# Kernel optimization log

Measured on AMD Instinct MI355X. Metric: run time of the kernel, lower is better.

Reference implementation:

```python
import jax, jax.numpy as jnp
import numpy as np

N_NODES = 100000
D_IN = 256
D_HID = 64
D_EMB = 32
ADJ_NNZ = 3200000
N_EDGES = 2000000


def setup_inputs() -> dict:
    key = jax.random.key(0)
    ks = jax.random.split(key, 8)
    x = jax.random.normal(ks[0], (N_NODES, D_IN), dtype=jnp.float32)
    adj_src = jax.random.randint(ks[1], (ADJ_NNZ,), 0, N_NODES, dtype=jnp.int32)
    adj_dst = jax.random.randint(ks[2], (ADJ_NNZ,), 0, N_NODES, dtype=jnp.int32)
    adj_val = jax.random.uniform(ks[3], (ADJ_NNZ,), dtype=jnp.float32)
    edge_index = jax.random.randint(ks[4], (2, N_EDGES), 0, N_NODES, dtype=jnp.int32)
    # Xavier-uniform weights, zero biases (matches reset_parameters)
    lim1 = float(np.sqrt(6.0 / (D_IN + D_HID)))
    lim2 = float(np.sqrt(6.0 / (D_HID + D_EMB)))
    W1 = jax.random.uniform(ks[5], (D_IN, D_HID), minval=-lim1, maxval=lim1, dtype=jnp.float32)
    b1 = jnp.zeros((D_HID,), dtype=jnp.float32)
    W2 = jax.random.uniform(ks[6], (D_HID, D_EMB), minval=-lim2, maxval=lim2, dtype=jnp.float32)
    b2 = jnp.zeros((D_EMB,), dtype=jnp.float32)
    return {"x": x, "adj_src": adj_src, "adj_dst": adj_dst, "adj_val": adj_val,
            "edge_index": edge_index, "W1": W1, "b1": b1, "W2": W2, "b2": b2}


def _spmm(adj_src, adj_dst, adj_val, dense):
    # (sparse A) @ dense : out[i] = sum_{e: dst[e]==i} val[e] * dense[src[e]]
    n = dense.shape[0]
    msgs = adj_val[:, None] * dense[adj_src]            # [nnz, d]
    return jax.ops.segment_sum(msgs, adj_dst, num_segments=n)


def reference(x, adj_src, adj_dst, adj_val, edge_index, W1, b1, W2, b2):
    # Layer 1: ReLU(A_norm @ (x W1) + b1)
    z1 = jax.nn.relu(_spmm(adj_src, adj_dst, adj_val, x @ W1) + b1)
    # Layer 2: A_norm @ (z1 W2) + b2 (no activation)
    z2 = _spmm(adj_src, adj_dst, adj_val, z1 @ W2) + b2   # [n, d_emb]
    # Inner-product decoder over edges
    src, dst = edge_index[0], edge_index[1]
    scores = jnp.sum(z2[src] * z2[dst], axis=1)          # [num_edges]
    return scores
```

## Files before the change

### kernel.cpp

```cpp
#include <hip/hip_runtime.h>
#include <hip/hip_bf16.h>


#define D_IN  256
#define D_HID 64
#define D_EMB 32
#define BROWS 256
#define NBUK_MAX 512
#define TILE  4096
#define PBS   512
#define SBS   1024

typedef unsigned short u16;
typedef unsigned int u32;
typedef __attribute__((ext_vector_type(8))) short short8;
typedef __attribute__((ext_vector_type(4))) float f32x4;

__device__ __forceinline__ float bf2f(u32 u) {
  return __uint_as_float((u & 0xFFFFu) << 16);
}
__device__ __forceinline__ float bf2f_hi(u32 u) {
  return __uint_as_float(u & 0xFFFF0000u);
}
__device__ __forceinline__ u16 f2bf(float f) {
  u32 x = __float_as_uint(f);
  x += 0x7FFFu + ((x >> 16) & 1u);
  return (u16)(x >> 16);
}
__device__ __forceinline__ void unpack8(uint4 u, float* f) {
  f[0] = bf2f(u.x); f[1] = bf2f(u.x >> 16);
  f[2] = bf2f(u.y); f[3] = bf2f(u.y >> 16);
  f[4] = bf2f(u.z); f[5] = bf2f(u.z >> 16);
  f[6] = bf2f(u.w); f[7] = bf2f(u.w >> 16);
}

__global__ __launch_bounds__(256) void w1_swizzle_kernel(
    const float* __restrict__ W1, uint4* __restrict__ gswz) {
  const int s = blockIdx.x * 256 + threadIdx.x;
  const int lane = s & 63;
  const int kstep = (s >> 6) & 7;
  const int nt = s >> 9;
  const int col = nt * 16 + (lane & 15);
  const int kbase = kstep * 32 + (lane >> 4) * 8;
  u32 p[4];
  for (int jp = 0; jp < 4; ++jp) {
    u32 lo = f2bf(W1[(kbase + 2 * jp) * D_HID + col]);
    u32 hi = f2bf(W1[(kbase + 2 * jp + 1) * D_HID + col]);
    p[jp] = lo | (hi << 16);
  }
  gswz[s] = make_uint4(p[0], p[1], p[2], p[3]);
}

__global__ __launch_bounds__(256) void gemm1_mfma_kernel(
    const float* __restrict__ x, const uint4* __restrict__ gswz,
    u16* __restrict__ h1, int M) {
  const int tid = threadIdx.x;
  const int wv = tid >> 6;
  const int lane = tid & 63;
  const int quad = lane >> 4;
  const int m = lane & 15;

  const int rowbase = blockIdx.x * 64 + wv * 16;
  int arow = rowbase + m;
  if (arow >= M) arow = M - 1;

  f32x4 acc[4];
  for (int nt = 0; nt < 4; ++nt) acc[nt] = (f32x4){0.f, 0.f, 0.f, 0.f};

  const float* xrow = &x[(long long)arow * D_IN];

#pragma unroll
  for (int kstep = 0; kstep < 8; ++kstep) {
    const int kbase = kstep * 32 + quad * 8;
    float4 a0 = *(const float4*)&xrow[kbase];
    float4 a1 = *(const float4*)&xrow[kbase + 4];
    short8 af;
    af[0] = (short)f2bf(a0.x); af[1] = (short)f2bf(a0.y);
    af[2] = (short)f2bf(a0.z); af[3] = (short)f2bf(a0.w);
    af[4] = (short)f2bf(a1.x); af[5] = (short)f2bf(a1.y);
    af[6] = (short)f2bf(a1.z); af[7] = (short)f2bf(a1.w);
#pragma unroll
    for (int nt = 0; nt < 4; ++nt) {
      uint4 bu = gswz[(nt * 8 + kstep) * 64 + lane];
      short8 bf = *(short8*)&bu;
      acc[nt] = __builtin_amdgcn_mfma_f32_16x16x32_bf16(af, bf, acc[nt], 0, 0, 0);
    }
  }

#pragma unroll
  for (int nt = 0; nt < 4; ++nt) {
#pragma unroll
    for (int r = 0; r < 4; ++r) {
      int orow = rowbase + quad * 4 + r;
      if (orow < M)
        h1[(long long)orow * D_HID + nt * 16 + m] = f2bf(acc[nt][r]);
    }
  }
}

__global__ __launch_bounds__(256) void bin_count(
    const int* __restrict__ dst, int* __restrict__ hist, int nnz, int nbuk) {
  __shared__ int h[NBUK_MAX];
  for (int i = threadIdx.x; i < nbuk; i += 256) h[i] = 0;
  __syncthreads();
  const int stride = gridDim.x * 256;
  for (int e = blockIdx.x * 256 + threadIdx.x; e < nnz; e += stride)
    atomicAdd(&h[dst[e] >> 8], 1);
  __syncthreads();
  for (int i = threadIdx.x; i < nbuk; i += 256) {
    int v = h[i];
    if (v) atomicAdd(&hist[i], v);
  }
}

__global__ __launch_bounds__(256) void bin_scan(
    int* __restrict__ hist, int* __restrict__ cur, int n) {
  __shared__ int sm[256];
  const int t = threadIdx.x;
  const int per = (n + 255) / 256;
  const int base = t * per;
  int loc[4];
  int s = 0;
  for (int i = 0; i < per; ++i) {
    int idx = base + i;
    int v = (idx < n) ? hist[idx] : 0;
    loc[i] = s;
    s += v;
  }
  sm[t] = s;
  __syncthreads();
  for (int off = 1; off < 256; off <<= 1) {
    int tmp = (t >= off) ? sm[t - off] : 0;
    __syncthreads();
    sm[t] += tmp;
    __syncthreads();
  }
  const int b0 = sm[t] - s;
  for (int i = 0; i < per; ++i) {
    int idx = base + i;
    if (idx < n) {
      int p = b0 + loc[i];
      hist[idx] = p;
      cur[idx] = p;
    }
  }
  if (t == 255) hist[n] = sm[255];
}

__global__ __launch_bounds__(PBS) void partition_kernel(
    const int* __restrict__ src, const int* __restrict__ dst,
    const float* __restrict__ val, int* __restrict__ cur,
    int2* __restrict__ payload, int nnz, int nbuk) {
  __shared__ int2 stage[TILE];
  __shared__ int hist[NBUK_MAX];
  __shared__ int lcur[NBUK_MAX];
  __shared__ int gbase[NBUK_MAX];
  __shared__ int sm[PBS];

  const int t = threadIdx.x;
  const long long base = (long long)blockIdx.x * TILE;
  const int cnt = min(TILE, (int)(nnz - base));

  for (int i = t; i < nbuk; i += PBS) hist[i] = 0;
  __syncthreads();

  constexpr int PER = TILE / PBS;
  int key[PER], vq[PER];
  short bk[PER];
  for (int i = 0; i < PER; ++i) {
    int idx = t + i * PBS;
    if (idx < cnt) {
      int d = dst[base + idx];
      int b = d >> 8;
      bk[i] = (short)b;
      key[i] = (src[base + idx] << 8) | (d & (BROWS - 1));
      int q = (int)(val[base + idx] * 32768.f + 0.5f);
      q = min(q, 32767);
      vq[i] = (b << 15) | q;
      atomicAdd(&hist[b], 1);
    } else {
      bk[i] = -1;
    }
  }
  __syncthreads();

  {
    int c = (t < nbuk) ? hist[t] : 0;
    sm[t] = c;
    __syncthreads();
    for (int off = 1; off < PBS; off <<= 1) {
      int tmp = (t >= off) ? sm[t - off] : 0;
      __syncthreads();
      sm[t] += tmp;
      __syncthreads();
    }
    int excl = sm[t] - c;
    if (t < nbuk) {
      hist[t] = excl;
      lcur[t] = excl;
      if (c > 0) gbase[t] = atomicAdd(&cur[t], c);
    }
  }
  __syncthreads();

  for (int i = 0; i < PER; ++i) {
    if (bk[i] >= 0) {
      int p = atomicAdd(&lcur[bk[i]], 1);
      stage[p] = make_int2(key[i], vq[i]);
    }
  }
  __syncthreads();

  for (int i = t; i < cnt; i += PBS) {
    int2 pk = stage[i];
    int b = pk.y >> 15;
    payload[gbase[b] + (i - hist[b])] = pk;
  }
}

__global__ __launch_bounds__(SBS) void bucket_sort_kernel(
    const int* __restrict__ bscan, const int2* __restrict__ payload,
    u32* __restrict__ csr, int* __restrict__ rs, int M) {
  __shared__ int cnt_s[BROWS];
  __shared__ int sm[BROWS];
  const int b = blockIdx.x;
  const int t = threadIdx.x;
  const int start = bscan[b];
  const int end = bscan[b + 1];

  if (t < BROWS) cnt_s[t] = 0;
  __syncthreads();
  for (int j = start + t; j < end; j += SBS)
    atomicAdd(&cnt_s[payload[j].x & (BROWS - 1)], 1);
  __syncthreads();

  int v = 0;
  if (t < BROWS) { v = cnt_s[t]; sm[t] = v; }
  __syncthreads();
  for (int off = 1; off < BROWS; off <<= 1) {
    int tmp = 0;
    if (t < BROWS && t >= off) tmp = sm[t - off];
    __syncthreads();
    if (t < BROWS) sm[t] += tmp;
    __syncthreads();
  }
  if (t < BROWS) {
    int row = b * BROWS + t;
    if (row < M) rs[row] = start + sm[t];
    cnt_s[t] = start + sm[t] - v;
  }
  __syncthreads();

  for (int j = start + t; j < end; j += SBS) {
    int2 pk = payload[j];
    int r = pk.x & (BROWS - 1);
    int p = atomicAdd(&cnt_s[r], 1);
    csr[p] = ((u32)(pk.x >> 8) << 15) | (u32)(pk.y & 32767);
  }
}

template <int D, bool RELU>
__global__ __launch_bounds__(256) void spmm_csr_kernel(
    const int* __restrict__ rs, const u32* __restrict__ csr,
    const u16* __restrict__ in, const float* __restrict__ bias,
    u16* __restrict__ out, int M) {
  constexpr int TEAM = D / 4;
  const int lt = threadIdx.x % TEAM;
  const int row = blockIdx.x * (256 / TEAM) + threadIdx.x / TEAM;
  if (row >= M) return;
  const int start = (row == 0) ? 0 : rs[row - 1];
  const int end = rs[row];
  const float qs = 1.f / 32768.f;
  const u16* inp = in + lt * 4;

  float a0 = 0.f, a1 = 0.f, a2 = 0.f, a3 = 0.f;
  int j = start;
  for (; j + 4 <= end; j += 4) {
    u32 p0 = csr[j], p1 = csr[j + 1], p2 = csr[j + 2], p3 = csr[j + 3];
    uint2 w0 = *(const uint2*)&inp[(long long)(p0 >> 15) * D];
    uint2 w1 = *(const uint2*)&inp[(long long)(p1 >> 15) * D];
    uint2 w2 = *(const uint2*)&inp[(long long)(p2 >> 15) * D];
    uint2 w3 = *(const uint2*)&inp[(long long)(p3 >> 15) * D];
    float v0 = (float)(p0 & 32767u) * qs;
    float v1 = (float)(p1 & 32767u) * qs;
    float v2 = (float)(p2 & 32767u) * qs;
    float v3 = (float)(p3 & 32767u) * qs;
    a0 = fmaf(v0, bf2f(w0.x), a0); a1 = fmaf(v0, bf2f_hi(w0.x), a1);
    a2 = fmaf(v0, bf2f(w0.y), a2); a3 = fmaf(v0, bf2f_hi(w0.y), a3);
    a0 = fmaf(v1, bf2f(w1.x), a0); a1 = fmaf(v1, bf2f_hi(w1.x), a1);
    a2 = fmaf(v1, bf2f(w1.y), a2); a3 = fmaf(v1, bf2f_hi(w1.y), a3);
    a0 = fmaf(v2, bf2f(w2.x), a0); a1 = fmaf(v2, bf2f_hi(w2.x), a1);
    a2 = fmaf(v2, bf2f(w2.y), a2); a3 = fmaf(v2, bf2f_hi(w2.y), a3);
    a0 = fmaf(v3, bf2f(w3.x), a0); a1 = fmaf(v3, bf2f_hi(w3.x), a1);
    a2 = fmaf(v3, bf2f(w3.y), a2); a3 = fmaf(v3, bf2f_hi(w3.y), a3);
  }
  for (; j < end; ++j) {
    u32 pk = csr[j];
    uint2 w = *(const uint2*)&inp[(long long)(pk >> 15) * D];
    float v = (float)(pk & 32767u) * qs;
    a0 = fmaf(v, bf2f(w.x), a0); a1 = fmaf(v, bf2f_hi(w.x), a1);
    a2 = fmaf(v, bf2f(w.y), a2); a3 = fmaf(v, bf2f_hi(w.y), a3);
  }
  const float4 bv = *(const float4*)&bias[lt * 4];
  a0 += bv.x; a1 += bv.y; a2 += bv.z; a3 += bv.w;
  if (RELU) {
    a0 = fmaxf(a0, 0.f); a1 = fmaxf(a1, 0.f);
    a2 = fmaxf(a2, 0.f); a3 = fmaxf(a3, 0.f);
  }
  uint2 o;
  o.x = (u32)f2bf(a0) | ((u32)f2bf(a1) << 16);
  o.y = (u32)f2bf(a2) | ((u32)f2bf(a3) << 16);
  *(uint2*)&out[(long long)row * D + lt * 4] = o;
}

__global__ __launch_bounds__(256) void gemm2_kernel(
    const u16* __restrict__ z1, const float* __restrict__ W2,
    u16* __restrict__ h2, int M) {
  __shared__ float ws[D_HID * D_EMB];
  const int tid = threadIdx.x;
  for (int i = tid; i < D_HID * D_EMB / 4; i += 256)
    ((float4*)ws)[i] = ((const float4*)W2)[i];
  __syncthreads();

  const int row = blockIdx.x * 256 + tid;
  if (row >= M) return;

  float4 acc4[8];
  for (int c = 0; c < 8; ++c) acc4[c] = make_float4(0.f, 0.f, 0.f, 0.f);

  const uint4* zr = (const uint4*)&z1[(long long)row * D_HID];
  for (int blk = 0; blk < 8; ++blk) {
    float a8[8];
    unpack8(zr[blk], a8);
    for (int kk = 0; kk < 8; ++kk) {
      const float a = a8[kk];
      const float4* wr = (const float4*)&ws[(blk * 8 + kk) * D_EMB];
      for (int c = 0; c < 8; ++c) {
        float4 wv = wr[c];
        acc4[c].x += a * wv.x;
        acc4[c].y += a * wv.y;
        acc4[c].z += a * wv.z;
        acc4[c].w += a * wv.w;
      }
    }
  }
  u32 pk[16];
  for (int c = 0; c < 8; ++c) {
    pk[c * 2 + 0] = (u32)f2bf(acc4[c].x) | ((u32)f2bf(acc4[c].y) << 16);
    pk[c * 2 + 1] = (u32)f2bf(acc4[c].z) | ((u32)f2bf(acc4[c].w) << 16);
  }
  uint4* op = (uint4*)&h2[(long long)row * D_EMB];
  op[0] = make_uint4(pk[0], pk[1], pk[2], pk[3]);
  op[1] = make_uint4(pk[4], pk[5], pk[6], pk[7]);
  op[2] = make_uint4(pk[8], pk[9], pk[10], pk[11]);
  op[3] = make_uint4(pk[12], pk[13], pk[14], pk[15]);
}

__global__ __launch_bounds__(256) void decode_kernel(
    const int* __restrict__ ei, const u16* __restrict__ z2,
    float* __restrict__ out, int nE) {
  const int e = blockIdx.x * 256 + threadIdx.x;
  if (e >= nE) return;
  const int s = ei[e];
  const int d = ei[nE + e];
  const uint4* za = (const uint4*)&z2[(long long)s * D_EMB];
  const uint4* zb = (const uint4*)&z2[(long long)d * D_EMB];
  float acc = 0.f;
  for (int c = 0; c < 4; ++c) {
    float a8[8], b8[8];
    unpack8(za[c], a8);
    unpack8(zb[c], b8);
    for (int k = 0; k < 8; ++k) acc = fmaf(a8[k], b8[k], acc);
  }
  out[e] = acc;
}

extern "C" void kernel_launch(void* const* d_in, const int* in_sizes, int n_in,
                              void* d_out, int out_size, void* d_ws, size_t ws_size,
                              hipStream_t stream) {
  const float* x       = (const float*)d_in[0];
  const int*   adj_src = (const int*)d_in[1];
  const int*   adj_dst = (const int*)d_in[2];
  const float* adj_val = (const float*)d_in[3];
  const int*   ei      = (const int*)d_in[4];
  const float* W1      = (const float*)d_in[5];
  const float* b1      = (const float*)d_in[6];
  const float* W2      = (const float*)d_in[7];
  const float* b2      = (const float*)d_in[8];

  const int M   = in_sizes[0] / D_IN;
  const int nnz = in_sizes[1];
  const int nE  = in_sizes[4] / 2;

  const int NBUK = (M + BROWS - 1) / BROWS;

  char* ws = (char*)d_ws;
  u32*   csr     = (u32*)(ws);
  int2*  payload = (int2*)(ws + (size_t)nnz * 4);
  u16*   h1      = (u16*)(ws + (size_t)nnz * 4);
  u16*   z1      = (u16*)(ws + (size_t)nnz * 4 + (size_t)nnz * 8);
  u16*   h2      = h1;
  u16*   z2      = z1;
  uint4* gswz    = (uint4*)(ws + 60ull * 1024 * 1024);

  int* rs    = (int*)d_out;
  int* bscan = (int*)d_out + 112 * 1024;
  int* cur   = (int*)d_out + 120 * 1024;

  w1_swizzle_kernel<<<8, 256, 0, stream>>>(W1, gswz);

  hipMemsetAsync(bscan, 0, (size_t)(NBUK + 1) * 4, stream);
  bin_count<<<256, 256, 0, stream>>>(adj_dst, bscan, nnz, NBUK);
  bin_scan<<<1, 256, 0, stream>>>(bscan, cur, NBUK);
  partition_kernel<<<(nnz + TILE - 1) / TILE, PBS, 0, stream>>>(
      adj_src, adj_dst, adj_val, cur, payload, nnz, NBUK);

  bucket_sort_kernel<<<NBUK, SBS, 0, stream>>>(bscan, payload, csr, rs, M);

  gemm1_mfma_kernel<<<(M + 63) / 64, 256, 0, stream>>>(x, gswz, h1, M);

  spmm_csr_kernel<D_HID, true><<<(M + 15) / 16, 256, 0, stream>>>(
      rs, csr, h1, b1, z1, M);

  gemm2_kernel<<<(M + 255) / 256, 256, 0, stream>>>(z1, W2, h2, M);

  spmm_csr_kernel<D_EMB, false><<<(M + 31) / 32, 256, 0, stream>>>(
      rs, csr, h2, b2, z2, M);

  decode_kernel<<<(nE + 255) / 256, 256, 0, stream>>>(ei, z2, (float*)d_out, nE);
}
```

Baseline: 431.9 us.

## Replace two-pass bucket sort CSR build with atomic histogram, scan, and scatter

```diff
diff --git a/kernel.cpp b/kernel.cpp
--- a/kernel.cpp
+++ b/kernel.cpp
@@ -5,11 +5,7 @@
 #define D_IN  256
 #define D_HID 64
 #define D_EMB 32
-#define BROWS 256
-#define NBUK_MAX 512
-#define TILE  4096
-#define PBS   512
-#define SBS   1024
+#define SCAN_ELEMS 1024
 
 typedef unsigned short u16;
 typedef unsigned int u32;
@@ -49,6 +45,122 @@
     p[jp] = lo | (hi << 16);
   }
   gswz[s] = make_uint4(p[0], p[1], p[2], p[3]);
+}
+
+__global__ __launch_bounds__(256) void hist_kernel(
+    const int* __restrict__ dst, int* __restrict__ rowcnt, int nnz) {
+  const int stride = gridDim.x * 256;
+  const int n4 = nnz >> 2;
+  const int4* d4 = (const int4*)dst;
+  for (int i = blockIdx.x * 256 + threadIdx.x; i < n4; i += stride) {
+    int4 d = d4[i];
+    atomicAdd(&rowcnt[d.x], 1);
+    atomicAdd(&rowcnt[d.y], 1);
+    atomicAdd(&rowcnt[d.z], 1);
+    atomicAdd(&rowcnt[d.w], 1);
+  }
+  for (int e = (n4 << 2) + blockIdx.x * 256 + threadIdx.x; e < nnz; e += stride)
+    atomicAdd(&rowcnt[dst[e]], 1);
+}
+
+__global__ __launch_bounds__(256) void scan_blocksum_kernel(
+    const int* __restrict__ rowcnt, int* __restrict__ bsum, int M) {
+  __shared__ int sm[256];
+  const int t = threadIdx.x;
+  const int base = blockIdx.x * SCAN_ELEMS + t * 4;
+  int s = 0;
+  if (base + 3 < M) {
+    int4 v = *(const int4*)&rowcnt[base];
+    s = v.x + v.y + v.z + v.w;
+  } else {
+    for (int i = 0; i < 4; ++i)
+      if (base + i < M) s += rowcnt[base + i];
+  }
+  sm[t] = s;
+  __syncthreads();
+  for (int off = 128; off > 0; off >>= 1) {
+    if (t < off) sm[t] += sm[t + off];
+    __syncthreads();
+  }
+  if (t == 0) bsum[blockIdx.x] = sm[0];
+}
+
+__global__ __launch_bounds__(256) void scan_write_kernel(
+    const int* __restrict__ rowcnt, const int* __restrict__ bsum,
+    int* __restrict__ rs, int* __restrict__ cur, int M, int NB) {
+  __shared__ int sm[256];
+  __shared__ int sbase;
+  const int t = threadIdx.x;
+  const int b = blockIdx.x;
+
+  int v = (t < b && t < NB) ? bsum[t] : 0;
+  sm[t] = v;
+  __syncthreads();
+  for (int off = 128; off > 0; off >>= 1) {
+    if (t < off) sm[t] += sm[t + off];
+    __syncthreads();
+  }
+  if (t == 0) sbase = sm[0];
+  __syncthreads();
+
+  const int base = b * SCAN_ELEMS + t * 4;
+  int c[4];
+  int s = 0;
+  for (int i = 0; i < 4; ++i) {
+    int idx = base + i;
+    c[i] = (idx < M) ? rowcnt[idx] : 0;
+    s += c[i];
+  }
+  sm[t] = s;
+  __syncthreads();
+  for (int off = 1; off < 256; off <<= 1) {
+    int tmp = (t >= off) ? sm[t - off] : 0;
+    __syncthreads();
+    sm[t] += tmp;
+    __syncthreads();
+  }
+  int start = sbase + sm[t] - s;
+  for (int i = 0; i < 4; ++i) {
+    int idx = base + i;
+    if (idx < M) {
+      cur[idx] = start;
+      start += c[i];
+      rs[idx] = start;
+    }
+  }
+}
+
+__global__ __launch_bounds__(256) void scatter_kernel(
+    const int* __restrict__ src, const int* __restrict__ dst,
+    const float* __restrict__ val, int* __restrict__ cur,
+    u32* __restrict__ csr, int nnz) {
+  const int stride = gridDim.x * 256;
+  const int n4 = nnz >> 2;
+  const int4* s4 = (const int4*)src;
+  const int4* d4 = (const int4*)dst;
+  const float4* v4 = (const float4*)val;
+  for (int i = blockIdx.x * 256 + threadIdx.x; i < n4; i += stride) {
+    int4 s = s4[i];
+    int4 d = d4[i];
+    float4 v = v4[i];
+    int q0 = min((int)(v.x * 32768.f + 0.5f), 32767);
+    int q1 = min((int)(v.y * 32768.f + 0.5f), 32767);
+    int q2 = min((int)(v.z * 32768.f + 0.5f), 32767);
+    int q3 = min((int)(v.w * 32768.f + 0.5f), 32767);
+    int p0 = atomicAdd(&cur[d.x], 1);
+    int p1 = atomicAdd(&cur[d.y], 1);
+    int p2 = atomicAdd(&cur[d.z], 1);
+    int p3 = atomicAdd(&cur[d.w], 1);
+    csr[p0] = ((u32)s.x << 15) | (u32)q0;
+    csr[p1] = ((u32)s.y << 15) | (u32)q1;
+    csr[p2] = ((u32)s.z << 15) | (u32)q2;
+    csr[p3] = ((u32)s.w << 15) | (u32)q3;
+  }
+  for (int e = (n4 << 2) + blockIdx.x * 256 + threadIdx.x; e < nnz; e += stride) {
+    int q = min((int)(val[e] * 32768.f + 0.5f), 32767);
+    int p = atomicAdd(&cur[dst[e]], 1);
+    csr[p] = ((u32)src[e] << 15) | (u32)q;
+  }
 }
 
 __global__ __launch_bounds__(256) void gemm1_mfma_kernel(
@@ -95,167 +207,6 @@
       if (orow < M)
         h1[(long long)orow * D_HID + nt * 16 + m] = f2bf(acc[nt][r]);
     }
-  }
-}
-
-__global__ __launch_bounds__(256) void bin_count(
-    const int* __restrict__ dst, int* __restrict__ hist, int nnz, int nbuk) {
-  __shared__ int h[NBUK_MAX];
-  for (int i = threadIdx.x; i < nbuk; i += 256) h[i] = 0;
-  __syncthreads();
-  const int stride = gridDim.x * 256;
-  for (int e = blockIdx.x * 256 + threadIdx.x; e < nnz; e += stride)
-    atomicAdd(&h[dst[e] >> 8], 1);
-  __syncthreads();
-  for (int i = threadIdx.x; i < nbuk; i += 256) {
-    int v = h[i];
-    if (v) atomicAdd(&hist[i], v);
-  }
-}
-
-__global__ __launch_bounds__(256) void bin_scan(
-    int* __restrict__ hist, int* __restrict__ cur, int n) {
-  __shared__ int sm[256];
-  const int t = threadIdx.x;
-  const int per = (n + 255) / 256;
-  const int base = t * per;
-  int loc[4];
-  int s = 0;
-  for (int i = 0; i < per; ++i) {
-    int idx = base + i;
-    int v = (idx < n) ? hist[idx] : 0;
-    loc[i] = s;
-    s += v;
-  }
-  sm[t] = s;
-  __syncthreads();
-  for (int off = 1; off < 256; off <<= 1) {
-    int tmp = (t >= off) ? sm[t - off] : 0;
-    __syncthreads();
-    sm[t] += tmp;
-    __syncthreads();
-  }
-  const int b0 = sm[t] - s;
-  for (int i = 0; i < per; ++i) {
-    int idx = base + i;
-    if (idx < n) {
-      int p = b0 + loc[i];
-      hist[idx] = p;
-      cur[idx] = p;
-    }
-  }
-  if (t == 255) hist[n] = sm[255];
-}
-
-__global__ __launch_bounds__(PBS) void partition_kernel(
-    const int* __restrict__ src, const int* __restrict__ dst,
-    const float* __restrict__ val, int* __restrict__ cur,
-    int2* __restrict__ payload, int nnz, int nbuk) {
-  __shared__ int2 stage[TILE];
-  __shared__ int hist[NBUK_MAX];
-  __shared__ int lcur[NBUK_MAX];
-  __shared__ int gbase[NBUK_MAX];
-  __shared__ int sm[PBS];
-
-  const int t = threadIdx.x;
-  const long long base = (long long)blockIdx.x * TILE;
-  const int cnt = min(TILE, (int)(nnz - base));
-
-  for (int i = t; i < nbuk; i += PBS) hist[i] = 0;
-  __syncthreads();
-
-  constexpr int PER = TILE / PBS;
-  int key[PER], vq[PER];
-  short bk[PER];
-  for (int i = 0; i < PER; ++i) {
-    int idx = t + i * PBS;
-    if (idx < cnt) {
-      int d = dst[base + idx];
-      int b = d >> 8;
-      bk[i] = (short)b;
-      key[i] = (src[base + idx] << 8) | (d & (BROWS - 1));
-      int q = (int)(val[base + idx] * 32768.f + 0.5f);
-      q = min(q, 32767);
-      vq[i] = (b << 15) | q;
-      atomicAdd(&hist[b], 1);
-    } else {
-      bk[i] = -1;
-    }
-  }
-  __syncthreads();
-
-  {
-    int c = (t < nbuk) ? hist[t] : 0;
-    sm[t] = c;
-    __syncthreads();
-    for (int off = 1; off < PBS; off <<= 1) {
-      int tmp = (t >= off) ? sm[t - off] : 0;
-      __syncthreads();
-      sm[t] += tmp;
-      __syncthreads();
-    }
-    int excl = sm[t] - c;
-    if (t < nbuk) {
-      hist[t] = excl;
-      lcur[t] = excl;
-      if (c > 0) gbase[t] = atomicAdd(&cur[t], c);
-    }
-  }
-  __syncthreads();
-
-  for (int i = 0; i < PER; ++i) {
-    if (bk[i] >= 0) {
-      int p = atomicAdd(&lcur[bk[i]], 1);
-      stage[p] = make_int2(key[i], vq[i]);
-    }
-  }
-  __syncthreads();
-
-  for (int i = t; i < cnt; i += PBS) {
-    int2 pk = stage[i];
-    int b = pk.y >> 15;
-    payload[gbase[b] + (i - hist[b])] = pk;
-  }
-}
-
-__global__ __launch_bounds__(SBS) void bucket_sort_kernel(
-    const int* __restrict__ bscan, const int2* __restrict__ payload,
-    u32* __restrict__ csr, int* __restrict__ rs, int M) {
-  __shared__ int cnt_s[BROWS];
-  __shared__ int sm[BROWS];
-  const int b = blockIdx.x;
-  const int t = threadIdx.x;
-  const int start = bscan[b];
-  const int end = bscan[b + 1];
-
-  if (t < BROWS) cnt_s[t] = 0;
-  __syncthreads();
-  for (int j = start + t; j < end; j += SBS)
-    atomicAdd(&cnt_s[payload[j].x & (BROWS - 1)], 1);
-  __syncthreads();
-
-  int v = 0;
-  if (t < BROWS) { v = cnt_s[t]; sm[t] = v; }
-  __syncthreads();
-  for (int off = 1; off < BROWS; off <<= 1) {
-    int tmp = 0;
-    if (t < BROWS && t >= off) tmp = sm[t - off];
-    __syncthreads();
-    if (t < BROWS) sm[t] += tmp;
-    __syncthreads();
-  }
-  if (t < BROWS) {
-    int row = b * BROWS + t;
-    if (row < M) rs[row] = start + sm[t];
-    cnt_s[t] = start + sm[t] - v;
-  }
-  __syncthreads();
-
-  for (int j = start + t; j < end; j += SBS) {
-    int2 pk = payload[j];
-    int r = pk.x & (BROWS - 1);
-    int p = atomicAdd(&cnt_s[r], 1);
-    csr[p] = ((u32)(pk.x >> 8) << 15) | (u32)(pk.y & 32767);
   }
 }
 
@@ -316,10 +267,10 @@
 __global__ __launch_bounds__(256) void gemm2_kernel(
     const u16* __restrict__ z1, const float* __restrict__ W2,
     u16* __restrict__ h2, int M) {
-  __shared__ float ws[D_HID * D_EMB];
+  __shared__ float wsm[D_HID * D_EMB];
   const int tid = threadIdx.x;
   for (int i = tid; i < D_HID * D_EMB / 4; i += 256)
-    ((float4*)ws)[i] = ((const float4*)W2)[i];
+    ((float4*)wsm)[i] = ((const float4*)W2)[i];
   __syncthreads();
 
   const int row = blockIdx.x * 256 + tid;
@@ -334,7 +285,7 @@
     unpack8(zr[blk], a8);
     for (int kk = 0; kk < 8; ++kk) {
       const float a = a8[kk];
-      const float4* wr = (const float4*)&ws[(blk * 8 + kk) * D_EMB];
+      const float4* wr = (const float4*)&wsm[(blk * 8 + kk) * D_EMB];
       for (int c = 0; c < 8; ++c) {
         float4 wv = wr[c];
         acc4[c].x += a * wv.x;
@@ -392,30 +343,28 @@
   const int nnz = in_sizes[1];
   const int nE  = in_sizes[4] / 2;
 
-  const int NBUK = (M + BROWS - 1) / BROWS;
+  const int NB = (M + SCAN_ELEMS - 1) / SCAN_ELEMS;
 
   char* ws = (char*)d_ws;
-  u32*   csr     = (u32*)(ws);
-  int2*  payload = (int2*)(ws + (size_t)nnz * 4);
-  u16*   h1      = (u16*)(ws + (size_t)nnz * 4);
-  u16*   z1      = (u16*)(ws + (size_t)nnz * 4 + (size_t)nnz * 8);
-  u16*   h2      = h1;
-  u16*   z2      = z1;
-  uint4* gswz    = (uint4*)(ws + 60ull * 1024 * 1024);
-
-  int* rs    = (int*)d_out;
-  int* bscan = (int*)d_out + 112 * 1024;
-  int* cur   = (int*)d_out + 120 * 1024;
+  u32*   csr  = (u32*)(ws);
+  u16*   h1   = (u16*)(ws + (size_t)nnz * 4);
+  u16*   z1   = (u16*)(ws + (size_t)nnz * 4 + (size_t)M * D_HID * 2);
+  u16*   h2   = h1;
+  u16*   z2   = z1;
+  uint4* gswz = (uint4*)(ws + 60ull * 1024 * 1024);
+
+  int* rs     = (int*)d_out;
+  int* rowcnt = (int*)d_out + 128 * 1024;
+  int* cur    = (int*)d_out + 256 * 1024;
+  int* bsum   = (int*)d_out + 384 * 1024;
 
   w1_swizzle_kernel<<<8, 256, 0, stream>>>(W1, gswz);
 
-  hipMemsetAsync(bscan, 0, (size_t)(NBUK + 1) * 4, stream);
-  bin_count<<<256, 256, 0, stream>>>(adj_dst, bscan, nnz, NBUK);
-  bin_scan<<<1, 256, 0, stream>>>(bscan, cur, NBUK);
-  partition_kernel<<<(nnz + TILE - 1) / TILE, PBS, 0, stream>>>(
-      adj_src, adj_dst, adj_val, cur, payload, nnz, NBUK);
-
-  bucket_sort_kernel<<<NBUK, SBS, 0, stream>>>(bscan, payload, csr, rs, M);
+  hipMemsetAsync(rowcnt, 0, (size_t)M * 4, stream);
+  hist_kernel<<<2048, 256, 0, stream>>>(adj_dst, rowcnt, nnz);
+  scan_blocksum_kernel<<<NB, 256, 0, stream>>>(rowcnt, bsum, M);
+  scan_write_kernel<<<NB, 256, 0, stream>>>(rowcnt, bsum, rs, cur, M, NB);
+  scatter_kernel<<<2048, 256, 0, stream>>>(adj_src, adj_dst, adj_val, cur, csr, nnz);
 
   gemm1_mfma_kernel<<<(M + 63) / 64, 256, 0, stream>>>(x, gswz, h1, M);
 
```

Result: slower. 705.3 us (+63.3%).
